# Optimization experiments

Measured on AMD Instinct MI355X. Metric: run time of the kernel, lower is better.

Reference implementation:

```python
import jax, jax.numpy as jnp
import numpy as np

L = 8          # layers_num
G = 2 * L + 1  # grid side = 17
NH = 30        # n_hiper
D = 768
N = 4096       # ray samples


def setup_inputs() -> dict:
    key = jax.random.key(0)
    k1, k2, k3 = jax.random.split(key, 3)
    # coords must be in [-L, L) so shifted indices floor+1/ceil+1 stay in-bounds
    samples = jax.random.uniform(k1, (N, 3), minval=-float(L), maxval=float(L) - 1e-3)
    last_point = jax.random.uniform(k2, (3,), minval=-float(L), maxval=float(L) - 1e-3)
    embeddings = jax.random.normal(k3, (G, G, G, NH + 1, D), dtype=jnp.float32)
    return {"samples": samples, "last_point": last_point, "embeddings": embeddings}


def _interpolate(emb, samples):
    """Vectorized port of Text3DSpaceAll.interpolate for all N samples.
    emb: (G,G,G,NH+1,D); samples: (N,3). Returns (N, NH+1, D)."""
    Gs = emb.shape[0]
    p = samples + L                       # shift into [0, G-1)
    f = jnp.floor(p)
    c = jnp.ceil(p)
    d = p - f                             # fractional parts (same as pre-shift)
    fx, fy, fz = f[:, 0].astype(jnp.int32), f[:, 1].astype(jnp.int32), f[:, 2].astype(jnp.int32)
    cy, cz = c[:, 1].astype(jnp.int32), c[:, 2].astype(jnp.int32)
    dx, dy, dz = d[:, 0], d[:, 1], d[:, 2]

    def w(a):  # broadcast per-sample scalar over (NH+1, D)
        return a[:, None, None]

    def clip(i):
        return jnp.clip(i, 0, Gs - 1)

    def line(iy, iz):
        # 2-4 point stencil along x with boundary-dependent count
        g = lambda ix: emb[clip(ix), iy, iz]          # gather -> (N, NH+1, D)
        m_lo = (fx > 0).astype(dx.dtype)
        m_hi = (fx + 2 < Gs).astype(dx.dtype)
        out = (g(fx) * w(2.0 - dx) + g(fx + 1) * w(1.0 + dx)
               + g(fx - 1) * w((1.0 - dx) * m_lo)
               + g(fx + 2) * w(dx * m_hi))
        cnt = 2.0 + m_lo + m_hi
        return out / w(cnt)

    def plane(iz):
        m_lo = (fy > 0).astype(dy.dtype)
        m_hi = (fy + 2 < Gs).astype(dy.dtype)
        out = (line(fy, iz) * w(2.0 - dy) + line(cy, iz) * w(1.0 + dy)
               + line(clip(fy - 1), iz) * w((1.0 - dy) * m_lo)
               + line(clip(cy + 1), iz) * w(dy * m_hi))
        cnt = 2.0 + m_lo + m_hi
        return out / w(cnt)

    m_lo = (fz > 0).astype(dz.dtype)
    m_hi = (fz + 2 < Gs).astype(dz.dtype)
    out = (plane(fz) * w(2.0 - dz) + plane(cz) * w(1.0 + dz)
           + plane(clip(fz - 1)) * w((1.0 - dz) * m_lo)
           + plane(clip(cz + 1)) * w(dz * m_hi))
    cnt = 2.0 + m_lo + m_hi
    return out / w(cnt)


def reference(samples, last_point, embeddings):
    n_hiper = embeddings.shape[3] - 1
    interp = _interpolate(embeddings, samples)          # (N, NH+1, D)
    emb = interp[:, :n_hiper]                           # (N, NH, D)
    density = jax.nn.relu(interp[:, n_hiper])           # (N, D)
    # distance from each sample to the next (last one to last_point)
    nxt = jnp.concatenate([samples[1:], last_point[None]], axis=0)
    dists = jnp.linalg.norm(samples - nxt, axis=-1)     # (N,)
    sd = density * dists[:, None]                       # (N, D)
    # exclusive cumulative optical depth -> transmittance
    csum = jnp.cumsum(sd, axis=0)
    excl = jnp.concatenate([jnp.zeros_like(sd[:1]), csum[:-1]], axis=0)
    T = jnp.exp(-excl)
    alpha = 1.0 - jnp.exp(-sd)
    wgt = T * alpha                                     # (N, D)
    return jnp.einsum('nd,nhd->hd', wgt, emb)           # (NH, D)
```

## Files before the change

### kernel.cpp

```cpp
#include <hip/hip_runtime.h>
#include <math.h>

#define LL 8
#define G 17
#define NH 30
#define D 768
#define N 4096
#define CH 31
#define CELLS (G*G*G)
#define CSTRIDE (CH*D)
#define NBIN 16
#define CPG 16
#define NCHUNK ((CELLS+CPG-1)/CPG)

__device__ __forceinline__ int iclip(int i){ return i<0?0:(i>G-1?G-1:i); }

__global__ void k_prep(const float* __restrict__ samples, const float* __restrict__ last_point,
                       float* __restrict__ wxyz, int* __restrict__ ixyz,
                       float* __restrict__ dist, int* __restrict__ sampleBin,
                       int* __restrict__ binCount){
    int s = blockIdx.x*blockDim.x + threadIdx.x;
    if (s >= N) return;
    float x0 = samples[s*3+0], y0 = samples[s*3+1], z0 = samples[s*3+2];
    float p[3] = {x0 + (float)LL, y0 + (float)LL, z0 + (float)LL};
    float fv[3], cv[3], dv[3]; int fi[3], ci[3];
    for (int a=0;a<3;a++){
        fv[a]=floorf(p[a]); cv[a]=ceilf(p[a]); dv[a]=p[a]-fv[a];
        fi[a]=(int)fv[a]; ci[a]=(int)cv[a];
    }
    {
        int fx=fi[0]; float dx=dv[0];
        float mlo=(fx>0)?1.f:0.f, mhi=(fx+2<G)?1.f:0.f;
        float cnt=2.f+mlo+mhi;
        float w[4]={(1.f-dx)*mlo/cnt,(2.f-dx)/cnt,(1.f+dx)/cnt,dx*mhi/cnt};
        int id[4]={iclip(fx-1),iclip(fx),iclip(fx+1),iclip(fx+2)};
        for(int i=0;i<4;i++){ wxyz[s*12+i]=w[i]; ixyz[s*12+i]=id[i]; }
    }
    {
        int fy=fi[1], cy=ci[1]; float dy=dv[1];
        float mlo=(fy>0)?1.f:0.f, mhi=(fy+2<G)?1.f:0.f;
        float cnt=2.f+mlo+mhi;
        float w[4]={(1.f-dy)*mlo/cnt,(2.f-dy)/cnt,(1.f+dy)/cnt,dy*mhi/cnt};
        int id[4]={iclip(fy-1),iclip(fy),iclip(cy),iclip(cy+1)};
        for(int i=0;i<4;i++){ wxyz[s*12+4+i]=w[i]; ixyz[s*12+4+i]=id[i]; }
    }
    {
        int fz=fi[2], cz=ci[2]; float dz=dv[2];
        float mlo=(fz>0)?1.f:0.f, mhi=(fz+2<G)?1.f:0.f;
        float cnt=2.f+mlo+mhi;
        float w[4]={(1.f-dz)*mlo/cnt,(2.f-dz)/cnt,(1.f+dz)/cnt,dz*mhi/cnt};
        int id[4]={iclip(fz-1),iclip(fz),iclip(cz),iclip(cz+1)};
        for(int i=0;i<4;i++){ wxyz[s*12+8+i]=w[i]; ixyz[s*12+8+i]=id[i]; }
    }
    float nx,ny,nz;
    if (s < N-1){ nx=samples[(s+1)*3+0]; ny=samples[(s+1)*3+1]; nz=samples[(s+1)*3+2]; }
    else        { nx=last_point[0];      ny=last_point[1];      nz=last_point[2]; }
    float ddx=x0-nx, ddy=y0-ny, ddz=z0-nz;
    dist[s]=sqrtf(ddx*ddx+ddy*ddy+ddz*ddz);
    int bx=min(max(fi[0],0),NBIN-1), by=min(max(fi[1],0),NBIN-1), bz=min(max(fi[2],0),NBIN-1);
    int bin=(bz*NBIN+by)*NBIN+bx;
    sampleBin[s]=bin;
    atomicAdd(&binCount[bin],1);
}

__global__ void k_binscan(const int* __restrict__ binCount, int* __restrict__ binStart,
                          int* __restrict__ binCursor){
    __shared__ int sh[256];
    __shared__ int srun;
    int t = threadIdx.x;
    if (t==0) srun=0;
    __syncthreads();
    for (int base=0; base<NBIN*NBIN*NBIN; base+=256){
        int v = binCount[base+t];
        sh[t]=v; __syncthreads();
        for (int off=1; off<256; off<<=1){
            int u = (t>=off)? sh[t-off] : 0;
            __syncthreads();
            sh[t]+=u;
            __syncthreads();
        }
        int incl = sh[t];
        int st = srun + incl - v;
        binStart[base+t]=st; binCursor[base+t]=st;
        __syncthreads();
        if (t==255) srun += incl;
        __syncthreads();
    }
}

__global__ void k_scatter(const int* __restrict__ sampleBin, int* __restrict__ binCursor,
                          int* __restrict__ binned){
    int s = blockIdx.x*blockDim.x + threadIdx.x;
    if (s>=N) return;
    int b=sampleBin[s];
    int pos=atomicAdd(&binCursor[b],1);
    binned[pos]=s;
}

__global__ __launch_bounds__(192) void k_density(const float* __restrict__ emb,
                       const float* __restrict__ wxyz, const int* __restrict__ ixyz,
                       const int* __restrict__ binned,
                       float* __restrict__ density){
    int b = blockIdx.x;
    int s = binned[((b & 7) << 9) | (b >> 3)];
    int t = threadIdx.x;
    __shared__ float w[12]; __shared__ int idx[12];
    __shared__ float lw[64]; __shared__ int loff[64];
    __shared__ int lcnt;
    if (t<12){ w[t]=wxyz[s*12+t]; idx[t]=ixyz[s*12+t]; }
    if (t==0) lcnt=0;
    __syncthreads();
    if (t < 64){
        int i = t>>4, j = (t>>2)&3, k = t&3;
        float www = w[i]*w[4+j]*w[8+k];
        if (www != 0.f){
            int pos = atomicAdd(&lcnt, 1);
            lw[pos]   = www;
            loff[pos] = ((idx[i]*G+idx[4+j])*G+idx[8+k])*CSTRIDE + NH*D;
        }
    }
    __syncthreads();
    int m = lcnt;
    float4 acc = make_float4(0.f,0.f,0.f,0.f);
    #pragma unroll 4
    for (int q=0;q<m;q++){
        const float4* p = (const float4*)(emb + (size_t)loff[q]);
        float4 v = p[t];
        float www = lw[q];
        acc.x += www*v.x; acc.y += www*v.y; acc.z += www*v.z; acc.w += www*v.w;
    }
    ((float4*)(density + (size_t)s*D))[t] = acc;
}

__global__ void k_transpose(const float* __restrict__ in, float* __restrict__ out,
                            int R, int C){
    __shared__ float tile[64][65];
    int tx=threadIdx.x, ty=threadIdx.y;
    int c0=blockIdx.x*64, r0=blockIdx.y*64;
    #pragma unroll
    for (int k=0;k<16;k++){
        int r=r0+ty+k*4;
        tile[ty+k*4][tx] = in[(size_t)r*C + c0 + tx];
    }
    __syncthreads();
    #pragma unroll
    for (int k=0;k<16;k++){
        int c=c0+ty+k*4;
        out[(size_t)c*R + r0 + tx] = tile[tx][ty+k*4];
    }
}

#define SIDX(n) ((n) + ((n)>>4))
__global__ __launch_bounds__(256) void k_scan(const float* __restrict__ density_t,
                       const float* __restrict__ dist, float* __restrict__ wgt_t){
    __shared__ float buf[4096 + 256];
    __shared__ float wtot[4];
    int t = threadIdx.x;
    int d = blockIdx.x;
    const float* col = density_t + (size_t)d*N;
    float* out = wgt_t + (size_t)d*N;
    #pragma unroll
    for (int i=0;i<16;i++){
        int n = i*256 + t;
        buf[SIDX(n)] = fmaxf(col[n], 0.f) * dist[n];
    }
    __syncthreads();
    int lane = t & 63, wave = t >> 6;
    float vals[16]; float sum = 0.f;
    #pragma unroll
    for (int j=0;j<16;j++){ vals[j] = buf[SIDX(t*16+j)]; sum += vals[j]; }
    float x = sum;
    #pragma unroll
    for (int off=1; off<64; off<<=1){
        float u = __shfl_up(x, (unsigned)off, 64);
        if (lane >= off) x += u;
    }
    if (lane == 63) wtot[wave] = x;
    float thread_excl = x - sum;
    __syncthreads();
    float wexcl = 0.f;
    for (int w2=0; w2<4; w2++) if (w2 < wave) wexcl += wtot[w2];
    float run = wexcl + thread_excl;
    #pragma unroll
    for (int j=0;j<16;j++){
        float sd = vals[j];
        run += sd;
        buf[SIDX(t*16+j)] = expf(sd-run) - expf(-run);
    }
    __syncthreads();
    #pragma unroll
    for (int i=0;i<16;i++){
        int n = i*256 + t;
        out[n] = buf[SIDX(n)];
    }
}

#define MAXS 1024
__global__ __launch_bounds__(192) void k_accumA(const float* __restrict__ wgt,
                       const float* __restrict__ wxyz, const int* __restrict__ ixyz,
                       const int* __restrict__ binStart, const int* __restrict__ binCount,
                       const int* __restrict__ binned, float* __restrict__ A){
    int b = blockIdx.x;
    int c = (b & 7) * 615 + (b >> 3);
    if (c >= CELLS) return;
    int t = threadIdx.x;
    int x=c/(G*G); int rem=c-x*G*G; int y=rem/G; int z=rem-y*G;
    __shared__ int   ls[MAXS];
    __shared__ float lw[MAXS];
    __shared__ int   lcount;
    if (t==0) lcount = 0;
    __syncthreads();
    int bx0=max(0,x-2), bx1=min(NBIN-1,x+1);
    int by0=max(0,y-2), by1=min(NBIN-1,y+1);
    int bz0=max(0,z-2), bz1=min(NBIN-1,z+1);
    int nx=bx1-bx0+1, ny=by1-by0+1, nz=bz1-bz0+1;
    int nb = nx*ny*nz;
    for (int bi=t; bi<nb; bi+=192){
        int bxo = bi % nx; int r2 = bi / nx;
        int byo = r2 % ny; int bzo = r2 / ny;
        int bin = ((bz0+bzo)*NBIN + (by0+byo))*NBIN + (bx0+bxo);
        int st = binStart[bin], cnt = binCount[bin];
        for (int q=0;q<cnt;q++){
            int s = binned[st+q];
            const float* w = wxyz + (size_t)s*12;
            const int* id  = ixyz + (size_t)s*12;
            float px=0.f,py=0.f,pz=0.f;
            #pragma unroll
            for (int i=0;i<4;i++){
                px += (id[i]  ==x)? w[i]  :0.f;
                py += (id[4+i]==y)? w[4+i]:0.f;
                pz += (id[8+i]==z)? w[8+i]:0.f;
            }
            float wt = px*py*pz;
            if (wt != 0.f){
                int pos = atomicAdd(&lcount, 1);
                if (pos < MAXS){ ls[pos]=s; lw[pos]=wt; }
            }
        }
    }
    __syncthreads();
    int m = min(lcount, MAXS);
    float4 acc = make_float4(0.f,0.f,0.f,0.f);
    for (int i=0;i<m;i++){
        int s = ls[i]; float wt = lw[i];
        float4 v = ((const float4*)(wgt + (size_t)s*D))[t];
        acc.x += wt*v.x; acc.y += wt*v.y; acc.z += wt*v.z; acc.w += wt*v.w;
    }
    ((float4*)(A + (size_t)c*D))[t] = acc;
}

__global__ __launch_bounds__(192) void k_out(const float* __restrict__ emb,
                      const float* __restrict__ A, float* __restrict__ partial){
    int t = threadIdx.x;
    int chunk = blockIdx.x;
    int h0 = blockIdx.y * 10;
    int c0 = chunk*CPG;
    int c1 = min(CELLS, c0+CPG);
    float4 acc[10];
    #pragma unroll
    for (int h=0;h<10;h++) acc[h]=make_float4(0.f,0.f,0.f,0.f);
    for (int c=c0;c<c1;c++){
        float4 a = ((const float4*)(A + (size_t)c*D))[t];
        const float* ebase = emb + (size_t)c*CSTRIDE + (size_t)h0*D;
        #pragma unroll
        for (int h=0;h<10;h++){
            float4 v = ((const float4*)(ebase + (size_t)h*D))[t];
            acc[h].x += a.x*v.x; acc[h].y += a.y*v.y;
            acc[h].z += a.z*v.z; acc[h].w += a.w*v.w;
        }
    }
    float* pr = partial + (size_t)chunk*NH*D + (size_t)h0*D;
    #pragma unroll
    for (int h=0;h<10;h++)
        ((float4*)(pr + (size_t)h*D))[t] = acc[h];
}

__global__ __launch_bounds__(256) void k_reduce(const float* __restrict__ partial,
                       float* __restrict__ out){
    int i = blockIdx.x*256 + threadIdx.x;
    if (i >= NH*D/4) return;
    int cbeg = blockIdx.y * 77;
    int cend = min(NCHUNK, cbeg + 77);
    float4 s = make_float4(0.f,0.f,0.f,0.f);
    #pragma unroll 4
    for (int c=cbeg;c<cend;c++){
        float4 v = ((const float4*)(partial + (size_t)c*NH*D))[i];
        s.x+=v.x; s.y+=v.y; s.z+=v.z; s.w+=v.w;
    }
    atomicAdd(&out[i*4+0], s.x);
    atomicAdd(&out[i*4+1], s.y);
    atomicAdd(&out[i*4+2], s.z);
    atomicAdd(&out[i*4+3], s.w);
}

extern "C" void kernel_launch(void* const* d_in, const int* in_sizes, int n_in,
                              void* d_out, int out_size, void* d_ws, size_t ws_size,
                              hipStream_t stream){
    const float* samples   = (const float*)d_in[0];
    const float* last_point= (const float*)d_in[1];
    const float* emb       = (const float*)d_in[2];
    char* ws=(char*)d_ws;
    float* wxyz     =(float*)(ws + 0);
    int*   ixyz     =(int*)  (ws + 196608);
    float* dist     =(float*)(ws + 393216);
    int*   sampleBin=(int*)  (ws + 409600);
    int*   binCount =(int*)  (ws + 425984);
    int*   binStart =(int*)  (ws + 442368);
    int*   binCursor=(int*)  (ws + 458752);
    int*   binned   =(int*)  (ws + 475136);
    float* density  =(float*)(ws + 524288);
    float* density_t=(float*)(ws + 524288 + 12582912);
    float* wgt_t    =(float*)(ws + 524288 + 2*12582912);
    float* wgt      = density;
    float* A        =(float*)(ws + 524288 + 3*12582912);
    float* partial  =(float*)(ws + 524288 + 3*12582912 + 15093504);

    hipMemsetAsync(binCount, 0, 4096*sizeof(int), stream);
    hipMemsetAsync(d_out, 0, NH*D*sizeof(float), stream);

    k_prep   <<<N/256, 256, 0, stream>>>(samples, last_point, wxyz, ixyz, dist, sampleBin, binCount);
    k_binscan<<<1, 256, 0, stream>>>(binCount, binStart, binCursor);
    k_scatter<<<N/256, 256, 0, stream>>>(sampleBin, binCursor, binned);
    k_density<<<N, 192, 0, stream>>>(emb, wxyz, ixyz, binned, density);
    dim3 tb(64,4);
    k_transpose<<<dim3(D/64, N/64), tb, 0, stream>>>(density, density_t, N, D);
    k_scan   <<<D, 256, 0, stream>>>(density_t, dist, wgt_t);
    k_transpose<<<dim3(N/64, D/64), tb, 0, stream>>>(wgt_t, wgt, D, N);
    k_accumA <<<8*615, 192, 0, stream>>>(wgt, wxyz, ixyz, binStart, binCount, binned, A);
    k_out    <<<dim3(NCHUNK, 3), 192, 0, stream>>>(emb, A, partial);
    k_reduce <<<dim3((NH*D/4+255)/256, 4), 256, 0, stream>>>(partial, (float*)d_out);
}
```

Baseline: 746.5 us.

## Tile density gather and A accumulation over 2x2x2 spatial blocks for reuse

The density kernel changes from one block per sample to one block per 2x2x2 group of bins. Each block loads the 5x5x5 neighbourhood of density embedding rows once and applies them to up to 8 samples at a time using per-axis weights kept in shared memory. The A-accumulation kernel likewise moves to one block per 2x2x2 cell group: each weight row it reads feeds 8 cell accumulators, with a shared-memory prefix scan used to gather candidate samples. This cuts redundant global and L2 reads, at the cost of far fewer blocks, serial bin gathering by one thread, and fixed capacity caps (128 and 512) that would silently drop samples in dense regions.

```diff
diff --git a/kernel.cpp b/kernel.cpp
--- a/kernel.cpp
+++ b/kernel.cpp
@@ -97,39 +97,80 @@
     binned[pos]=s;
 }
 
-__global__ __launch_bounds__(192) void k_density(const float* __restrict__ emb,
+#define MAXK 128
+__global__ __launch_bounds__(192) void k_density2(const float* __restrict__ emb,
                        const float* __restrict__ wxyz, const int* __restrict__ ixyz,
-                       const int* __restrict__ binned,
-                       float* __restrict__ density){
+                       const int* __restrict__ binStart, const int* __restrict__ binCount,
+                       const int* __restrict__ binned, float* __restrict__ density){
     int b = blockIdx.x;
-    int s = binned[((b & 7) << 9) | (b >> 3)];
+    int Bz = b & 7;
+    int rem = b >> 3;
+    int By = rem >> 3, Bx = rem & 7;
     int t = threadIdx.x;
-    __shared__ float w[12]; __shared__ int idx[12];
-    __shared__ float lw[64]; __shared__ int loff[64];
-    __shared__ int lcnt;
-    if (t<12){ w[t]=wxyz[s*12+t]; idx[t]=ixyz[s*12+t]; }
-    if (t==0) lcnt=0;
-    __syncthreads();
-    if (t < 64){
-        int i = t>>4, j = (t>>2)&3, k = t&3;
-        float www = w[i]*w[4+j]*w[8+k];
-        if (www != 0.f){
-            int pos = atomicAdd(&lcnt, 1);
-            lw[pos]   = www;
-            loff[pos] = ((idx[i]*G+idx[4+j])*G+idx[8+k])*CSTRIDE + NH*D;
-        }
-    }
-    __syncthreads();
-    int m = lcnt;
-    float4 acc = make_float4(0.f,0.f,0.f,0.f);
-    #pragma unroll 4
-    for (int q=0;q<m;q++){
-        const float4* p = (const float4*)(emb + (size_t)loff[q]);
-        float4 v = p[t];
-        float www = lw[q];
-        acc.x += www*v.x; acc.y += www*v.y; acc.z += www*v.z; acc.w += www*v.w;
-    }
-    ((float4*)(density + (size_t)s*D))[t] = acc;
+    __shared__ int   ssid[MAXK];
+    __shared__ float ws5[MAXK*15];
+    __shared__ int   sk;
+    if (t==0){
+        int k=0;
+        for (int dzb=0; dzb<2; dzb++)
+        for (int dyb=0; dyb<2; dyb++)
+        for (int dxb=0; dxb<2; dxb++){
+            int bin = ((2*Bz+dzb)*NBIN + (2*By+dyb))*NBIN + (2*Bx+dxb);
+            int st = binStart[bin], cnt = binCount[bin];
+            for (int q=0;q<cnt && k<MAXK;q++) ssid[k++] = binned[st+q];
+        }
+        sk = k;
+    }
+    __syncthreads();
+    int k = sk;
+    if (k==0) return;
+    int bx0 = 2*Bx-1, by0 = 2*By-1, bz0 = 2*Bz-1;
+    for (int u=t; u<k*15; u+=192){
+        int s = u/15, r = u - s*15, ax = r/5, pos = r - ax*5;
+        int X = ((ax==0)?bx0:(ax==1)?by0:bz0) + pos;
+        int sid = ssid[s];
+        const float* w = wxyz + (size_t)sid*12 + ax*4;
+        const int*  id = ixyz + (size_t)sid*12 + ax*4;
+        float a = 0.f;
+        #pragma unroll
+        for (int i=0;i<4;i++) a += (id[i]==X)? w[i] : 0.f;
+        ws5[u] = a;
+    }
+    __syncthreads();
+    for (int g0=0; g0<k; g0+=8){
+        int gn = min(8, k-g0);
+        float4 acc[8];
+        #pragma unroll
+        for (int s=0;s<8;s++) acc[s]=make_float4(0.f,0.f,0.f,0.f);
+        for (int z5=0; z5<5; z5++){
+            int Z = bz0+z5; if (Z<0 || Z>G-1) continue;
+            for (int y5=0; y5<5; y5++){
+                int Y = by0+y5; if (Y<0 || Y>G-1) continue;
+                float wyz[8];
+                #pragma unroll
+                for (int s=0;s<8;s++){
+                    int si = min(g0+s, k-1);
+                    wyz[s] = (s<gn)? ws5[si*15+5+y5]*ws5[si*15+10+z5] : 0.f;
+                }
+                for (int x5=0; x5<5; x5++){
+                    int X = bx0+x5; if (X<0 || X>G-1) continue;
+                    const float4* p = (const float4*)(emb + (size_t)((X*G+Y)*G+Z)*CSTRIDE + NH*D);
+                    float4 v = p[t];
+                    #pragma unroll
+                    for (int s=0;s<8;s++){
+                        int si = min(g0+s, k-1);
+                        float wc = wyz[s]*ws5[si*15+x5];
+                        acc[s].x += wc*v.x; acc[s].y += wc*v.y;
+                        acc[s].z += wc*v.z; acc[s].w += wc*v.w;
+                    }
+                }
+            }
+        }
+        #pragma unroll
+        for (int s=0;s<8;s++){
+            if (s<gn) ((float4*)(density + (size_t)ssid[g0+s]*D))[t] = acc[s];
+        }
+    }
 }
 
 __global__ void k_transpose(const float* __restrict__ in, float* __restrict__ out,
@@ -195,58 +236,90 @@
     }
 }
 
-#define MAXS 1024
-__global__ __launch_bounds__(192) void k_accumA(const float* __restrict__ wgt,
+#define MAXS2 512
+__global__ __launch_bounds__(192) void k_accumA2(const float* __restrict__ wgt,
                        const float* __restrict__ wxyz, const int* __restrict__ ixyz,
                        const int* __restrict__ binStart, const int* __restrict__ binCount,
                        const int* __restrict__ binned, float* __restrict__ A){
     int b = blockIdx.x;
-    int c = (b & 7) * 615 + (b >> 3);
-    if (c >= CELLS) return;
+    int CZ = b % 9; int r2 = b / 9; int CY = r2 % 9; int CX = r2 / 9;
+    int x0 = 2*CX, y0 = 2*CY, z0 = 2*CZ;
     int t = threadIdx.x;
-    int x=c/(G*G); int rem=c-x*G*G; int y=rem/G; int z=rem-y*G;
-    __shared__ int   ls[MAXS];
-    __shared__ float lw[MAXS];
-    __shared__ int   lcount;
-    if (t==0) lcount = 0;
-    __syncthreads();
-    int bx0=max(0,x-2), bx1=min(NBIN-1,x+1);
-    int by0=max(0,y-2), by1=min(NBIN-1,y+1);
-    int bz0=max(0,z-2), bz1=min(NBIN-1,z+1);
+    __shared__ int   ls[MAXS2];
+    __shared__ float lw6[MAXS2*6];
+    __shared__ int   bst[128];
+    __shared__ int   sc[128];
+    __shared__ int   own[128];
+    int bx0=max(0,x0-2), bx1=min(NBIN-1,x0+2);
+    int by0=max(0,y0-2), by1=min(NBIN-1,y0+2);
+    int bz0=max(0,z0-2), bz1=min(NBIN-1,z0+2);
     int nx=bx1-bx0+1, ny=by1-by0+1, nz=bz1-bz0+1;
     int nb = nx*ny*nz;
-    for (int bi=t; bi<nb; bi+=192){
-        int bxo = bi % nx; int r2 = bi / nx;
-        int byo = r2 % ny; int bzo = r2 / ny;
-        int bin = ((bz0+bzo)*NBIN + (by0+byo))*NBIN + (bx0+bxo);
-        int st = binStart[bin], cnt = binCount[bin];
-        for (int q=0;q<cnt;q++){
-            int s = binned[st+q];
-            const float* w = wxyz + (size_t)s*12;
-            const int* id  = ixyz + (size_t)s*12;
-            float px=0.f,py=0.f,pz=0.f;
-            #pragma unroll
-            for (int i=0;i<4;i++){
-                px += (id[i]  ==x)? w[i]  :0.f;
-                py += (id[4+i]==y)? w[4+i]:0.f;
-                pz += (id[8+i]==z)? w[8+i]:0.f;
-            }
-            float wt = px*py*pz;
-            if (wt != 0.f){
-                int pos = atomicAdd(&lcount, 1);
-                if (pos < MAXS){ ls[pos]=s; lw[pos]=wt; }
-            }
-        }
-    }
-    __syncthreads();
-    int m = min(lcount, MAXS);
-    float4 acc = make_float4(0.f,0.f,0.f,0.f);
-    for (int i=0;i<m;i++){
-        int s = ls[i]; float wt = lw[i];
-        float4 v = ((const float4*)(wgt + (size_t)s*D))[t];
-        acc.x += wt*v.x; acc.y += wt*v.y; acc.z += wt*v.z; acc.w += wt*v.w;
-    }
-    ((float4*)(A + (size_t)c*D))[t] = acc;
+    if (t<128){
+        int v=0, st=0;
+        if (t<nb){
+            int bx = t % nx; int rr = t / nx; int by = rr % ny; int bz = rr / ny;
+            int bin = ((bz0+bz)*NBIN + (by0+by))*NBIN + (bx0+bx);
+            st = binStart[bin]; v = binCount[bin];
+        }
+        bst[t]=st; own[t]=v; sc[t]=v;
+    }
+    __syncthreads();
+    for (int off=1; off<128; off<<=1){
+        int u = (t<128 && t>=off)? sc[t-off] : 0;
+        __syncthreads();
+        if (t<128) sc[t]+=u;
+        __syncthreads();
+    }
+    int k = min(sc[127], MAXS2);
+    for (int u=t; u<nb; u+=192){
+        int off = sc[u]-own[u], st = bst[u], c = own[u];
+        for (int q=0;q<c;q++) if (off+q < MAXS2) ls[off+q] = binned[st+q];
+    }
+    __syncthreads();
+    for (int u=t; u<k*6; u+=192){
+        int s = u/6, r = u - s*6, ax = r>>1, pos = r&1;
+        int X = ((ax==0)?x0:(ax==1)?y0:z0) + pos;
+        int sid = ls[s];
+        const float* w = wxyz + (size_t)sid*12 + ax*4;
+        const int*  id = ixyz + (size_t)sid*12 + ax*4;
+        float a = 0.f;
+        #pragma unroll
+        for (int i=0;i<4;i++) a += (id[i]==X)? w[i] : 0.f;
+        lw6[u] = a;
+    }
+    __syncthreads();
+    float4 acc[8];
+    #pragma unroll
+    for (int i=0;i<8;i++) acc[i]=make_float4(0.f,0.f,0.f,0.f);
+    for (int s=0;s<k;s++){
+        float4 v = ((const float4*)(wgt + (size_t)ls[s]*D))[t];
+        float wx0=lw6[s*6+0], wx1=lw6[s*6+1];
+        float wy0=lw6[s*6+2], wy1=lw6[s*6+3];
+        float wz0=lw6[s*6+4], wz1=lw6[s*6+5];
+        float wyz00=wy0*wz0, wyz10=wy1*wz0, wyz01=wy0*wz1, wyz11=wy1*wz1;
+        float wc;
+        wc=wx0*wyz00; acc[0].x+=wc*v.x; acc[0].y+=wc*v.y; acc[0].z+=wc*v.z; acc[0].w+=wc*v.w;
+        wc=wx1*wyz00; acc[1].x+=wc*v.x; acc[1].y+=wc*v.y; acc[1].z+=wc*v.z; acc[1].w+=wc*v.w;
+        wc=wx0*wyz10; acc[2].x+=wc*v.x; acc[2].y+=wc*v.y; acc[2].z+=wc*v.z; acc[2].w+=wc*v.w;
+        wc=wx1*wyz10; acc[3].x+=wc*v.x; acc[3].y+=wc*v.y; acc[3].z+=wc*v.z; acc[3].w+=wc*v.w;
+        wc=wx0*wyz01; acc[4].x+=wc*v.x; acc[4].y+=wc*v.y; acc[4].z+=wc*v.z; acc[4].w+=wc*v.w;
+        wc=wx1*wyz01; acc[5].x+=wc*v.x; acc[5].y+=wc*v.y; acc[5].z+=wc*v.z; acc[5].w+=wc*v.w;
+        wc=wx0*wyz11; acc[6].x+=wc*v.x; acc[6].y+=wc*v.y; acc[6].z+=wc*v.z; acc[6].w+=wc*v.w;
+        wc=wx1*wyz11; acc[7].x+=wc*v.x; acc[7].y+=wc*v.y; acc[7].z+=wc*v.z; acc[7].w+=wc*v.w;
+    }
+    #pragma unroll
+    for (int dz=0;dz<2;dz++)
+    #pragma unroll
+    for (int dy=0;dy<2;dy++)
+    #pragma unroll
+    for (int dx=0;dx<2;dx++){
+        int X=x0+dx, Y=y0+dy, Z=z0+dz;
+        if (X<G && Y<G && Z<G){
+            int c=(X*G+Y)*G+Z;
+            ((float4*)(A + (size_t)c*D))[t] = acc[dx+2*dy+4*dz];
+        }
+    }
 }
 
 __global__ __launch_bounds__(192) void k_out(const float* __restrict__ emb,
@@ -318,15 +391,15 @@
     hipMemsetAsync(binCount, 0, 4096*sizeof(int), stream);
     hipMemsetAsync(d_out, 0, NH*D*sizeof(float), stream);
 
-    k_prep   <<<N/256, 256, 0, stream>>>(samples, last_point, wxyz, ixyz, dist, sampleBin, binCount);
-    k_binscan<<<1, 256, 0, stream>>>(binCount, binStart, binCursor);
-    k_scatter<<<N/256, 256, 0, stream>>>(sampleBin, binCursor, binned);
-    k_density<<<N, 192, 0, stream>>>(emb, wxyz, ixyz, binned, density);
+    k_prep    <<<N/256, 256, 0, stream>>>(samples, last_point, wxyz, ixyz, dist, sampleBin, binCount);
+    k_binscan <<<1, 256, 0, stream>>>(binCount, binStart, binCursor);
+    k_scatter <<<N/256, 256, 0, stream>>>(sampleBin, binCursor, binned);
+    k_density2<<<512, 192, 0, stream>>>(emb, wxyz, ixyz, binStart, binCount, binned, density);
     dim3 tb(64,4);
     k_transpose<<<dim3(D/64, N/64), tb, 0, stream>>>(density, density_t, N, D);
-    k_scan   <<<D, 256, 0, stream>>>(density_t, dist, wgt_t);
+    k_scan    <<<D, 256, 0, stream>>>(density_t, dist, wgt_t);
     k_transpose<<<dim3(N/64, D/64), tb, 0, stream>>>(wgt_t, wgt, D, N);
-    k_accumA <<<8*615, 192, 0, stream>>>(wgt, wxyz, ixyz, binStart, binCount, binned, A);
-    k_out    <<<dim3(NCHUNK, 3), 192, 0, stream>>>(emb, A, partial);
-    k_reduce <<<dim3((NH*D/4+255)/256, 4), 256, 0, stream>>>(partial, (float*)d_out);
-}
+    k_accumA2 <<<729, 192, 0, stream>>>(wgt, wxyz, ixyz, binStart, binCount, binned, A);
+    k_out     <<<dim3(NCHUNK, 3), 192, 0, stream>>>(emb, A, partial);
+    k_reduce  <<<dim3((NH*D/4+255)/256, 4), 256, 0, stream>>>(partial, (float*)d_out);
+}
```

After: 778.1 us. 4.2% more time.
